# Kernel tuning notes

Hardware: AMD Instinct MI355X
Metric: run time of the kernel (lower is better)

The kernel has to match this reference:

```python
import jax, jax.numpy as jnp
import numpy as np

N_VARS = 32
D_MODEL = 256
D_MECH = 128
D_NOISE = D_MODEL // 4
N_LAYERS = 3
TEMP = 0.5
BATCH = 512


def gelu(x):
    return jax.nn.gelu(x, approximate=False)  # torch nn.GELU default is exact erf


def setup_inputs() -> dict:
    key = jax.random.key(0)
    ks = jax.random.split(key, 12)
    n, d, m, dn = N_VARS, D_MODEL, D_MECH, D_NOISE
    return {
        "exogenous_noise": jax.random.normal(ks[0], (BATCH, n, dn), dtype=jnp.float32),
        # learned params (edge_logits init randn*0.5 for a nontrivial adjacency)
        "edge_logits": jax.random.normal(ks[1], (n, n), dtype=jnp.float32) * 0.5,
        "var_emb": jax.random.normal(ks[2], (n, d), dtype=jnp.float32) * 0.02,
        # shared parent_aggregate Linear(d, d); weights stored [in, out]
        "pa_W": jax.random.normal(ks[3], (d, d), dtype=jnp.float32) / np.sqrt(d).astype(np.float32),
        "pa_b": jnp.zeros((d,), dtype=jnp.float32),
        # per-variable mechanism MLP weights, stacked on variable axis
        "m_W1": jax.random.normal(ks[4], (n, d, m), dtype=jnp.float32) / np.sqrt(d).astype(np.float32),
        "m_b1": jnp.zeros((n, m), dtype=jnp.float32),
        "m_W2": jax.random.normal(ks[5], (n, m, m), dtype=jnp.float32) / np.sqrt(m).astype(np.float32),
        "m_b2": jnp.zeros((n, m), dtype=jnp.float32),
        "m_W3": jax.random.normal(ks[6], (n, m, d), dtype=jnp.float32) / np.sqrt(m).astype(np.float32),
        "m_b3": jnp.zeros((n, d), dtype=jnp.float32),
        # per-variable noise encoder Linear(dn, d)
        "ne_W": jax.random.normal(ks[7], (n, dn, d), dtype=jnp.float32) / np.sqrt(dn).astype(np.float32),
        "ne_b": jnp.zeros((n, d), dtype=jnp.float32),
    }


def _forward(exogenous_noise, edge_logits, var_emb, pa_W, pa_b,
             m_W1, m_b1, m_W2, m_b2, m_W3, m_b3, ne_W, ne_b):
    n, d = N_VARS, D_MODEL
    batch = exogenous_noise.shape[0]
    # eval-mode adjacency: sigmoid(masked_logits / temp); diagonal masked out
    diag_mask = 1.0 - jnp.eye(n, dtype=edge_logits.dtype)
    adj = jax.nn.sigmoid((edge_logits * diag_mask) / jnp.asarray(TEMP, edge_logits.dtype))
    adj_cols = adj.T                                  # row i = adj[:, i], parents of var i
    noise_t = jnp.transpose(exogenous_noise, (1, 0, 2))  # (n, batch, dn)

    values0 = jnp.zeros((batch, n, d), dtype=exogenous_noise.dtype)
    idx = jnp.arange(n)
    xs = (idx, adj_cols, var_emb, noise_t, m_W1, m_b1, m_W2, m_b2, m_W3, m_b3, ne_W, ne_b)

    def var_step(values, x):
        i, a_col, emb_i, nz, w1, b1, w2, b2, w3, b3, nw, nb = x
        # adjacency-weighted aggregation over ALL current values (sequentially updated)
        pc = jnp.einsum('v,bvd->bd', a_col, values)
        parent_input = gelu((pc + emb_i) @ pa_W + pa_b)
        h = gelu(parent_input @ w1 + b1)
        h = gelu(h @ w2 + b2)
        out = h @ w3 + b3
        out = out + gelu(nz @ nw + nb)               # noise encoder contribution
        values = values.at[:, i].set(out)
        return values, None

    values = values0
    for _ in range(N_LAYERS):
        values, _ = jax.lax.scan(var_step, values, xs)
    return values


def reference(exogenous_noise, edge_logits, var_emb, pa_W, pa_b,
              m_W1, m_b1, m_W2, m_b2, m_W3, m_b3, ne_W, ne_b):
    return _forward(exogenous_noise, edge_logits, var_emb, pa_W, pa_b,
                    m_W1, m_b1, m_W2, m_b2, m_W3, m_b3, ne_W, ne_b)
```

## Files before the change

kernel.cpp:

```cpp
#include <hip/hip_runtime.h>


typedef __bf16 bf16x8 __attribute__((ext_vector_type(8)));
typedef float  f32x4  __attribute__((ext_vector_type(4)));

#define N_VARS 32
#define BTILE 4
#define NBLK 128

#define WS_ADJB   0
#define WS_B3P    4096
#define WS_EMBP   36864
#define WS_WSB    69632
#define ELOFF_PA  0
#define ELOFF_W1  65536
#define ELOFF_W2  1114112
#define ELOFF_W3  1638400
#define ELOFF_W3P 2686976
#define WS_H2B    7540736

#define XSTR 272
#define HSTR 144
#define VSTR 40

__device__ __forceinline__ unsigned short f2b(float f) {
    unsigned u = __float_as_uint(f);
    u += 0x7FFFu + ((u >> 16) & 1u);
    return (unsigned short)(u >> 16);
}

__device__ __forceinline__ float b2f(unsigned short u) {
    return __uint_as_float(((unsigned)u) << 16);
}

__device__ __forceinline__ void bar_lds() {
    asm volatile("s_waitcnt lgkmcnt(0)\n\ts_barrier" ::: "memory");
}

__device__ __forceinline__ float gelu_e(float x) {
    float z  = x * 0.7071067811865476f;
    float az = fabsf(z);
    float t  = __builtin_amdgcn_rcpf(1.0f + 0.47047f * az);
    float p  = t * (0.3480242f + t * (-0.0958798f + t * 0.7478556f));
    float e  = 1.0f - p * __expf(-z * z);
    float er = (z < 0.0f) ? -e : e;
    return 0.5f * x * (1.0f + er);
}

__device__ __forceinline__ float pickq(f32x4 v, int q) {
    float lo = (q & 1) ? v[1] : v[0];
    float hi = (q & 1) ? v[3] : v[2];
    return (q & 2) ? hi : lo;
}

#define MFMA16(a, b, c) __builtin_amdgcn_mfma_f32_16x16x32_bf16(a, b, c, 0, 0, 0)

#define GLD4(dst, ptr) asm volatile("global_load_dwordx4 %0, %1, off" \
                                    : "=v"(dst) : "v"(ptr))
#define GLD1(dst, ptr) asm volatile("global_load_dword %0, %1, off" \
                                    : "=v"(dst) : "v"(ptr))

__global__ void prep_all(const float* __restrict__ paW, const float* __restrict__ mW1,
                         const float* __restrict__ mW2, const float* __restrict__ mW3,
                         const float* __restrict__ edge, unsigned short* __restrict__ wsb,
                         unsigned short* __restrict__ adjb,
                         const float* __restrict__ noise, const float* __restrict__ neW,
                         const float* __restrict__ neb, float* __restrict__ outp,
                         const float* __restrict__ mb3, const float* __restrict__ emb,
                         const float* __restrict__ pab,
                         float* __restrict__ b3P, float* __restrict__ embP) {
    __shared__ unsigned short tile[32 * 256];
    const int c = blockIdx.x, tid = threadIdx.x;
    if (c < 520) {
        const float* src; unsigned short* dst; int N, KS, ks;
        if (c < 8)        { src = paW;                     dst = wsb + ELOFF_PA;             N = 256; KS = 8; ks = c; }
        else if (c < 264) { int v = (c - 8) >> 3;   ks = (c - 8) & 7;
                            src = mW1 + v * 32768;         dst = wsb + ELOFF_W1 + v * 32768; N = 128; KS = 8; }
        else if (c < 392) { int v = (c - 264) >> 2; ks = (c - 264) & 3;
                            src = mW2 + v * 16384;         dst = wsb + ELOFF_W2 + v * 16384; N = 128; KS = 4; }
        else              { int v = (c - 392) >> 2; ks = (c - 392) & 3;
                            src = mW3 + v * 32768;         dst = wsb + ELOFF_W3 + v * 32768; N = 256; KS = 4; }
        const int kb = ks * 32, nsh = (N == 256) ? 8 : 7;
        for (int t = tid; t < 32 * N; t += 256) {
            int r = t >> nsh, col = t & (N - 1);
            tile[r * N + col] = f2b(src[(kb + r) * N + col]);
        }
        __syncthreads();
        const int nout = (N >> 4) * 64;
        for (int o = tid; o < nout; o += 256) {
            int nt = o >> 6, lane = o & 63;
            int n = nt * 16 + (lane & 15), k0 = (lane >> 4) << 3;
            unsigned e[8];
            #pragma unroll
            for (int j = 0; j < 8; j++) e[j] = tile[(k0 + j) * N + n];
            uint4 pk;
            pk.x = e[0] | (e[1] << 16); pk.y = e[2] | (e[3] << 16);
            pk.z = e[4] | (e[5] << 16); pk.w = e[6] | (e[7] << 16);
            *(uint4*)(dst + ((nt * KS + ks) * 64 + lane) * 8) = pk;
        }
    } else if (c == 520) {
        for (int t = tid; t < 1024; t += 256) {
            int v = t >> 5, ci = t & 31;
            float x = edge[t];
            float m = (v == ci) ? 0.0f : x;
            float a = __builtin_amdgcn_rcpf(1.0f + __expf(-2.0f * m));
            unsigned short hi = f2b(a);
            float rem = a - b2f(hi);
            adjb[ci * 64 + v]      = hi;
            adjb[ci * 64 + 32 + v] = f2b(rem);
        }
    } else if (c < 1545) {
        int sb = c - 521;
        int i = sb >> 5, g = sb & 31, d = tid;
        float w[64];
        #pragma unroll
        for (int k = 0; k < 64; k++) w[k] = neW[(i * 64 + k) * 256 + d];
        float bias = neb[i * 256 + d];
        for (int bb = 0; bb < 16; bb++) {
            int b = g * 16 + bb;
            const float* nr = noise + (b * 32 + i) * 64;
            float a0 = bias, a1 = 0.f, a2 = 0.f, a3 = 0.f;
            #pragma unroll
            for (int k = 0; k < 16; k++) {
                a0 += nr[4 * k + 0] * w[4 * k + 0];
                a1 += nr[4 * k + 1] * w[4 * k + 1];
                a2 += nr[4 * k + 2] * w[4 * k + 2];
                a3 += nr[4 * k + 3] * w[4 * k + 3];
            }
            outp[(b * 32 + i) * 256 + d] = gelu_e((a0 + a1) + (a2 + a3));
        }
    } else if (c < 2057) {
        const int idx = c - 1545;
        const int v = idx >> 4, mg = (idx & 15) * 8;
        const int d = tid;
        const float* w3r = mW3 + (size_t)(v * 128 + mg) * 256;
        float acc[8];
        #pragma unroll
        for (int r = 0; r < 8; r++) acc[r] = 0.f;
        for (int n = 0; n < 256; n++) {
            float pa = paW[n * 256 + d];
            #pragma unroll
            for (int r = 0; r < 8; r++) acc[r] += w3r[r * 256 + n] * pa;
        }
        const int ks = mg >> 5, lg = (mg >> 3) & 3;
        const int nt = d >> 4, lane = lg * 16 + (d & 15);
        uint4 pk;
        pk.x = (unsigned)f2b(acc[0]) | ((unsigned)f2b(acc[1]) << 16);
        pk.y = (unsigned)f2b(acc[2]) | ((unsigned)f2b(acc[3]) << 16);
        pk.z = (unsigned)f2b(acc[4]) | ((unsigned)f2b(acc[5]) << 16);
        pk.w = (unsigned)f2b(acc[6]) | ((unsigned)f2b(acc[7]) << 16);
        *(uint4*)(wsb + ELOFF_W3P + v * 32768 + ((nt * 4 + ks) * 64 + lane) * 8) = pk;
    } else if (c < 2089) {
        const int v = c - 2057;
        float a = 0.f;
        for (int n = 0; n < 256; n++) a += mb3[v * 256 + n] * paW[n * 256 + tid];
        b3P[v * 256 + tid] = a;
    } else {
        const int v = c - 2089;
        float a = pab[tid];
        for (int n = 0; n < 256; n++) a += emb[v * 256 + n] * paW[n * 256 + tid];
        embP[v * 256 + tid] = a;
    }
}

__global__ __launch_bounds__(512, 2) void
scm_main(const float* __restrict__ embP, const float* __restrict__ b3Pp,
         const float* __restrict__ mb1, const float* __restrict__ mb2,
         const unsigned short* __restrict__ adjb,
         const __bf16* __restrict__ wsbf, const float* __restrict__ outp,
         unsigned short* __restrict__ h2buf) {
    __shared__ unsigned short valsP[1024 * VSTR];
    __shared__ unsigned short ne2S[4 * 32 * 256];
    __shared__ unsigned short adjS[2048];
    __shared__ unsigned short X2[4 * XSTR];
    __shared__ unsigned short Hs1[4 * HSTR];
    __shared__ unsigned short Hs2[4 * HSTR];

    const int tid = threadIdx.x, blk = blockIdx.x;

    {
        uint4 z; z.x = z.y = z.z = z.w = 0;
        for (int k = tid; k < 5120; k += 512) ((uint4*)valsP)[k] = z;
        for (int k = tid; k < 1024; k += 512)
            ((unsigned*)adjS)[k] = ((const unsigned*)adjb)[k];
    }

    const int wid = tid >> 6, lane = tid & 63, l15 = lane & 15, q = lane >> 4;
    const int l3 = l15 & 3;
    const int nW = wid * 16 + l15;
    const int n0 = nW, n1 = nW + 128;

    {
        const int R = wid * 16 + l15;
        const float* src = outp + ((size_t)(blk * BTILE + (R >> 5)) * 32 + (R & 31)) * 256 + q * 8;
        bf16x8 afr[8];
        #pragma unroll
        for (int ks = 0; ks < 8; ks++) {
            float4 x0 = *(const float4*)(src + ks * 32);
            float4 x1 = *(const float4*)(src + ks * 32 + 4);
            uint4 pk;
            pk.x = (unsigned)f2b(x0.x) | ((unsigned)f2b(x0.y) << 16);
            pk.y = (unsigned)f2b(x0.z) | ((unsigned)f2b(x0.w) << 16);
            pk.z = (unsigned)f2b(x1.x) | ((unsigned)f2b(x1.y) << 16);
            pk.w = (unsigned)f2b(x1.z) | ((unsigned)f2b(x1.w) << 16);
            afr[ks] = __builtin_bit_cast(bf16x8, pk);
        }
        #pragma unroll 4
        for (int nt = 0; nt < 16; nt++) {
            f32x4 e4 = {0, 0, 0, 0}, o4 = {0, 0, 0, 0};
            #pragma unroll
            for (int ks = 0; ks < 8; ks += 2) {
                bf16x8 b0 = *(const bf16x8*)(wsbf + ELOFF_PA + ((nt * 8 + ks) * 64 + lane) * 8);
                bf16x8 b1 = *(const bf16x8*)(wsbf + ELOFF_PA + ((nt * 8 + ks + 1) * 64 + lane) * 8);
                e4 = MFMA16(afr[ks], b0, e4);
                o4 = MFMA16(afr[ks + 1], b1, o4);
            }
            f32x4 a = e4 + o4;
            #pragma unroll
            for (int rr = 0; rr < 4; rr++) {
                int R2 = wid * 16 + q * 4 + rr;
                ne2S[R2 * 256 + nt * 16 + l15] =
                    f2b(a[rr] + b3Pp[(R2 & 31) * 256 + nt * 16 + l15]);
            }
        }
    }

    X2[q * XSTR + n0] = f2b(gelu_e(embP[n0]));
    X2[q * XSTR + n1] = f2b(gelu_e(embP[n1]));
    bar_lds();

    struct WSet {
        uint4 w1[8]; uint4 w2[4]; uint4 p0[4]; uint4 p1[4];
        float s0, s1, s2, s3;
    };

    auto issue_set = [&](WSet& S, int st) {
        const int it = st & 31, nt2 = (st + 1) & 31;
        const __bf16* b1 = wsbf + ELOFF_W1 + (size_t)it * 32768 +
                           ((size_t)(wid * 8) * 64 + lane) * 8;
        #pragma unroll
        for (int ks = 0; ks < 8; ks++) GLD4(S.w1[ks], b1 + ks * 512);
        const __bf16* b2 = wsbf + ELOFF_W2 + (size_t)it * 16384 +
                           ((size_t)(wid * 4) * 64 + lane) * 8;
        #pragma unroll
        for (int ks = 0; ks < 4; ks++) GLD4(S.w2[ks], b2 + ks * 512);
        const __bf16* bp = wsbf + ELOFF_W3P + (size_t)it * 32768 +
                           ((size_t)(wid * 4) * 64 + lane) * 8;
        #pragma unroll
        for (int ks = 0; ks < 4; ks++) GLD4(S.p0[ks], bp + ks * 512);
        const __bf16* bq = bp + 16384;
        #pragma unroll
        for (int ks = 0; ks < 4; ks++) GLD4(S.p1[ks], bq + ks * 512);
        GLD1(S.s0, mb1 + it * 128 + nW);
        GLD1(S.s1, mb2 + it * 128 + nW);
        GLD1(S.s2, embP + nt2 * 256 + n0);
        GLD1(S.s3, embP + nt2 * 256 + n1);
    };

    auto step = [&](int s, const WSet& cur, WSet& nxt) {
        const int i = s & 31, ni = (s + 1) & 31;
        const bool last = s >= 64;

        issue_set(nxt, s + 1);
        asm volatile("s_waitcnt vmcnt(24)");
        __builtin_amdgcn_sched_barrier(0);

        const float ne2_0 = b2f(ne2S[(q * 32 + i) * 256 + n0]);
        const float ne2_1 = b2f(ne2S[(q * 32 + i) * 256 + n1]);
        bf16x8 anh = *(const bf16x8*)(adjS + ni * 64 + q * 8);
        bf16x8 anl = *(const bf16x8*)(adjS + ni * 64 + 32 + q * 8);
        const float ani = b2f(adjS[ni * 64 + i]) + b2f(adjS[ni * 64 + 32 + i]);

        {
            f32x4 aa = {0, 0, 0, 0}, ab = {0, 0, 0, 0};
            f32x4 ac = {0, 0, 0, 0}, ad = {0, 0, 0, 0};
            #pragma unroll
            for (int ks = 0; ks < 8; ks += 4) {
                bf16x8 af0 = *(const bf16x8*)(X2 + l3 * XSTR + ks * 32 + q * 8);
                bf16x8 af1 = *(const bf16x8*)(X2 + l3 * XSTR + (ks + 1) * 32 + q * 8);
                bf16x8 af2 = *(const bf16x8*)(X2 + l3 * XSTR + (ks + 2) * 32 + q * 8);
                bf16x8 af3 = *(const bf16x8*)(X2 + l3 * XSTR + (ks + 3) * 32 + q * 8);
                aa = MFMA16(af0, __builtin_bit_cast(bf16x8, cur.w1[ks]), aa);
                ab = MFMA16(af1, __builtin_bit_cast(bf16x8, cur.w1[ks + 1]), ab);
                ac = MFMA16(af2, __builtin_bit_cast(bf16x8, cur.w1[ks + 2]), ac);
                ad = MFMA16(af3, __builtin_bit_cast(bf16x8, cur.w1[ks + 3]), ad);
            }
            float sb = (pickq(aa, q) + pickq(ab, q)) +
                       (pickq(ac, q) + pickq(ad, q)) + cur.s0;
            Hs1[q * HSTR + nW] = f2b(gelu_e(sb));
        }
        bar_lds();

        float pc0 = 0.f, pc1 = 0.f, oP0, oP1;
        {
            f32x4 ca = {0, 0, 0, 0}, cb = {0, 0, 0, 0};
            #pragma unroll
            for (int ks = 0; ks < 4; ks += 2) {
                bf16x8 af0 = *(const bf16x8*)(Hs1 + l3 * HSTR + ks * 32 + q * 8);
                bf16x8 af1 = *(const bf16x8*)(Hs1 + l3 * HSTR + (ks + 1) * 32 + q * 8);
                ca = MFMA16(af0, __builtin_bit_cast(bf16x8, cur.w2[ks]), ca);
                cb = MFMA16(af1, __builtin_bit_cast(bf16x8, cur.w2[ks + 1]), cb);
            }
            #pragma unroll
            for (int t = 0; t < 4; t++) {
                bf16x8 vf0 = *(const bf16x8*)(valsP + (t * 256 + n0) * VSTR + q * 8);
                bf16x8 vf1 = *(const bf16x8*)(valsP + (t * 256 + n1) * VSTR + q * 8);
                f32x4 z = {0, 0, 0, 0};
                f32x4 p0 = MFMA16(anl, vf0, MFMA16(anh, vf0, z));
                f32x4 p1 = MFMA16(anl, vf1, MFMA16(anh, vf1, z));
                pc0 = (q == t) ? p0[0] : pc0;
                pc1 = (q == t) ? p1[0] : pc1;
            }
            oP0 = b2f(valsP[(q * 256 + n0) * VSTR + i]);
            oP1 = b2f(valsP[(q * 256 + n1) * VSTR + i]);
            float scv = pickq(ca, q) + pickq(cb, q) + cur.s1;
            unsigned short hv = f2b(gelu_e(scv));
            Hs2[q * HSTR + nW] = hv;
            if (last)
                h2buf[((size_t)i * 512 + blk * BTILE + q) * 128 + nW] = hv;
        }
        bar_lds();

        {
            f32x4 c0a = {0, 0, 0, 0}, c0b = {0, 0, 0, 0};
            f32x4 c1a = {0, 0, 0, 0}, c1b = {0, 0, 0, 0};
            #pragma unroll
            for (int ks = 0; ks < 4; ks += 2) {
                bf16x8 af0 = *(const bf16x8*)(Hs2 + l3 * HSTR + ks * 32 + q * 8);
                bf16x8 af1 = *(const bf16x8*)(Hs2 + l3 * HSTR + (ks + 1) * 32 + q * 8);
                c0a = MFMA16(af0, __builtin_bit_cast(bf16x8, cur.p0[ks]), c0a);
                c1a = MFMA16(af0, __builtin_bit_cast(bf16x8, cur.p1[ks]), c1a);
                c0b = MFMA16(af1, __builtin_bit_cast(bf16x8, cur.p0[ks + 1]), c0b);
                c1b = MFMA16(af1, __builtin_bit_cast(bf16x8, cur.p1[ks + 1]), c1b);
            }
            float nP0 = pickq(c0a, q) + pickq(c0b, q) + ne2_0;
            float nP1 = pickq(c1a, q) + pickq(c1b, q) + ne2_1;
            unsigned short ur0 = f2b(nP0), ur1 = f2b(nP1);
            valsP[(q * 256 + n0) * VSTR + i] = ur0;
            valsP[(q * 256 + n1) * VSTR + i] = ur1;
            float x0 = pc0 + ani * (b2f(ur0) - oP0) + cur.s2;
            float x1 = pc1 + ani * (b2f(ur1) - oP1) + cur.s3;
            X2[q * XSTR + n0] = f2b(gelu_e(x0));
            X2[q * XSTR + n1] = f2b(gelu_e(x1));
        }
        bar_lds();
    };

    WSet A, B;
    issue_set(A, 0);
    asm volatile("s_waitcnt vmcnt(0)");
    __builtin_amdgcn_sched_barrier(0);
    for (int ss = 0; ss < 48; ss++) {
        step(2 * ss,     A, B);
        step(2 * ss + 1, B, A);
    }
}

__global__ __launch_bounds__(256) void
post_out(const unsigned short* __restrict__ h2buf, const __bf16* __restrict__ wsbf,
         const float* __restrict__ mb3, float* __restrict__ outp) {
    const int tid = threadIdx.x;
    const int wid = tid >> 6, lane = tid & 63, l15 = lane & 15, q = lane >> 4;
    const int gid = blockIdx.x * 4 + wid;
    const int i = gid >> 5, bt = gid & 31;
    bf16x8 af[4];
    #pragma unroll
    for (int ks = 0; ks < 4; ks++)
        af[ks] = *(const bf16x8*)(h2buf + ((size_t)i * 512 + bt * 16 + l15) * 128 +
                                  ks * 32 + q * 8);
    #pragma unroll 4
    for (int nt = 0; nt < 16; nt++) {
        f32x4 e4 = {0, 0, 0, 0}, o4 = {0, 0, 0, 0};
        #pragma unroll
        for (int ks = 0; ks < 4; ks += 2) {
            bf16x8 b0 = *(const bf16x8*)(wsbf + ELOFF_W3 + (size_t)i * 32768 +
                                         ((nt * 4 + ks) * 64 + lane) * 8);
            bf16x8 b1 = *(const bf16x8*)(wsbf + ELOFF_W3 + (size_t)i * 32768 +
                                         ((nt * 4 + ks + 1) * 64 + lane) * 8);
            e4 = MFMA16(af[ks], b0, e4);
            o4 = MFMA16(af[ks + 1], b1, o4);
        }
        f32x4 a = e4 + o4;
        float bv = mb3[i * 256 + nt * 16 + l15];
        #pragma unroll
        for (int rr = 0; rr < 4; rr++) {
            int b = bt * 16 + q * 4 + rr;
            size_t o = ((size_t)b * 32 + i) * 256 + nt * 16 + l15;
            outp[o] = a[rr] + bv + outp[o];
        }
    }
}

extern "C" void kernel_launch(void* const* d_in, const int* in_sizes, int n_in,
                              void* d_out, int out_size, void* d_ws, size_t ws_size,
                              hipStream_t stream) {
    (void)in_sizes; (void)n_in; (void)out_size; (void)ws_size;
    const float* noise = (const float*)d_in[0];
    const float* edge  = (const float*)d_in[1];
    const float* emb   = (const float*)d_in[2];
    const float* paW   = (const float*)d_in[3];
    const float* pab   = (const float*)d_in[4];
    const float* mW1   = (const float*)d_in[5];
    const float* mb1   = (const float*)d_in[6];
    const float* mW2   = (const float*)d_in[7];
    const float* mb2   = (const float*)d_in[8];
    const float* mW3   = (const float*)d_in[9];
    const float* mb3   = (const float*)d_in[10];
    const float* neW   = (const float*)d_in[11];
    const float* neb   = (const float*)d_in[12];
    float* outp = (float*)d_out;

    unsigned short* adjb = (unsigned short*)((char*)d_ws + WS_ADJB);
    float* b3P  = (float*)((char*)d_ws + WS_B3P);
    float* embP = (float*)((char*)d_ws + WS_EMBP);
    unsigned short* wsb  = (unsigned short*)((char*)d_ws + WS_WSB);
    unsigned short* h2b  = (unsigned short*)((char*)d_ws + WS_H2B);

    prep_all<<<2121, 256, 0, stream>>>(paW, mW1, mW2, mW3, edge, wsb, adjb,
                                       noise, neW, neb, outp, mb3, emb, pab,
                                       b3P, embP);
    scm_main<<<NBLK, 512, 0, stream>>>(embP, b3P, mb1, mb2, adjb,
                                       (const __bf16*)wsb, outp, h2b);
    post_out<<<256, 256, 0, stream>>>(h2b, (const __bf16*)wsb, mb3, outp);
}
```

Baseline: 386.4 us.

## Fuse final output projection into last layer of main recurrent kernel

Removes the separate post_out kernel and the h2buf staging buffer by computing the W3 projection, bias and noise-residual add inside scm_main's final-layer steps. The last 32 steps become an unpipelined loop that loads all weights, including W3, directly each step. This saves a launch and a global write/read of hidden states. In exchange it loses the weight prefetch overlap for those steps and raises register pressure.

```diff
diff --git a/kernel.cpp b/kernel.cpp
--- a/kernel.cpp
+++ b/kernel.cpp
@@ -17,7 +17,6 @@
 #define ELOFF_W2  1114112
 #define ELOFF_W3  1638400
 #define ELOFF_W3P 2686976
-#define WS_H2B    7540736
 
 #define XSTR 272
 #define HSTR 144
@@ -166,9 +165,8 @@
 __global__ __launch_bounds__(512, 2) void
 scm_main(const float* __restrict__ embP, const float* __restrict__ b3Pp,
          const float* __restrict__ mb1, const float* __restrict__ mb2,
-         const unsigned short* __restrict__ adjb,
-         const __bf16* __restrict__ wsbf, const float* __restrict__ outp,
-         unsigned short* __restrict__ h2buf) {
+         const float* __restrict__ mb3, const unsigned short* __restrict__ adjb,
+         const __bf16* __restrict__ wsbf, float* __restrict__ outp) {
     __shared__ unsigned short valsP[1024 * VSTR];
     __shared__ unsigned short ne2S[4 * 32 * 256];
     __shared__ unsigned short adjS[2048];
@@ -257,9 +255,8 @@
         GLD1(S.s3, embP + nt2 * 256 + n1);
     };
 
-    auto step = [&](int s, const WSet& cur, WSet& nxt) {
+    auto stepA = [&](int s, const WSet& cur, WSet& nxt) {
         const int i = s & 31, ni = (s + 1) & 31;
-        const bool last = s >= 64;
 
         issue_set(nxt, s + 1);
         asm volatile("s_waitcnt vmcnt(24)");
@@ -314,10 +311,7 @@
             oP0 = b2f(valsP[(q * 256 + n0) * VSTR + i]);
             oP1 = b2f(valsP[(q * 256 + n1) * VSTR + i]);
             float scv = pickq(ca, q) + pickq(cb, q) + cur.s1;
-            unsigned short hv = f2b(gelu_e(scv));
-            Hs2[q * HSTR + nW] = hv;
-            if (last)
-                h2buf[((size_t)i * 512 + blk * BTILE + q) * 128 + nW] = hv;
+            Hs2[q * HSTR + nW] = f2b(gelu_e(scv));
         }
         bar_lds();
 
@@ -350,44 +344,134 @@
     issue_set(A, 0);
     asm volatile("s_waitcnt vmcnt(0)");
     __builtin_amdgcn_sched_barrier(0);
-    for (int ss = 0; ss < 48; ss++) {
-        step(2 * ss,     A, B);
-        step(2 * ss + 1, B, A);
+    for (int ss = 0; ss < 32; ss++) {
+        stepA(2 * ss,     A, B);
+        stepA(2 * ss + 1, B, A);
     }
-}
-
-__global__ __launch_bounds__(256) void
-post_out(const unsigned short* __restrict__ h2buf, const __bf16* __restrict__ wsbf,
-         const float* __restrict__ mb3, float* __restrict__ outp) {
-    const int tid = threadIdx.x;
-    const int wid = tid >> 6, lane = tid & 63, l15 = lane & 15, q = lane >> 4;
-    const int gid = blockIdx.x * 4 + wid;
-    const int i = gid >> 5, bt = gid & 31;
-    bf16x8 af[4];
-    #pragma unroll
-    for (int ks = 0; ks < 4; ks++)
-        af[ks] = *(const bf16x8*)(h2buf + ((size_t)i * 512 + bt * 16 + l15) * 128 +
-                                  ks * 32 + q * 8);
-    #pragma unroll 4
-    for (int nt = 0; nt < 16; nt++) {
-        f32x4 e4 = {0, 0, 0, 0}, o4 = {0, 0, 0, 0};
-        #pragma unroll
-        for (int ks = 0; ks < 4; ks += 2) {
-            bf16x8 b0 = *(const bf16x8*)(wsbf + ELOFF_W3 + (size_t)i * 32768 +
-                                         ((nt * 4 + ks) * 64 + lane) * 8);
-            bf16x8 b1 = *(const bf16x8*)(wsbf + ELOFF_W3 + (size_t)i * 32768 +
-                                         ((nt * 4 + ks + 1) * 64 + lane) * 8);
-            e4 = MFMA16(af[ks], b0, e4);
-            o4 = MFMA16(af[ks + 1], b1, o4);
-        }
-        f32x4 a = e4 + o4;
-        float bv = mb3[i * 256 + nt * 16 + l15];
-        #pragma unroll
-        for (int rr = 0; rr < 4; rr++) {
-            int b = bt * 16 + q * 4 + rr;
-            size_t o = ((size_t)b * 32 + i) * 256 + nt * 16 + l15;
-            outp[o] = a[rr] + bv + outp[o];
-        }
+    asm volatile("s_waitcnt vmcnt(0)");
+    __builtin_amdgcn_sched_barrier(0);
+
+    for (int s = 64; s < 96; s++) {
+        const int i = s & 31, ni = (s + 1) & 31;
+
+        float bi1 = mb1[i * 128 + nW];
+        float bi2 = mb2[i * 128 + nW];
+        bf16x8 w1f[8];
+        #pragma unroll
+        for (int ks = 0; ks < 8; ks++)
+            w1f[ks] = *(const bf16x8*)(wsbf + ELOFF_W1 + (size_t)i * 32768 +
+                                       ((wid * 8 + ks) * 64 + lane) * 8);
+        bf16x8 w2f[4], wPf0[4], wPf1[4], w3f0[4], w3f1[4];
+        #pragma unroll
+        for (int ks = 0; ks < 4; ks++) {
+            w2f[ks]  = *(const bf16x8*)(wsbf + ELOFF_W2 + (size_t)i * 16384 +
+                                        ((wid * 4 + ks) * 64 + lane) * 8);
+            wPf0[ks] = *(const bf16x8*)(wsbf + ELOFF_W3P + (size_t)i * 32768 +
+                                        ((wid * 4 + ks) * 64 + lane) * 8);
+            wPf1[ks] = *(const bf16x8*)(wsbf + ELOFF_W3P + (size_t)i * 32768 +
+                                        (((wid + 8) * 4 + ks) * 64 + lane) * 8);
+            w3f0[ks] = *(const bf16x8*)(wsbf + ELOFF_W3 + (size_t)i * 32768 +
+                                        ((wid * 4 + ks) * 64 + lane) * 8);
+            w3f1[ks] = *(const bf16x8*)(wsbf + ELOFF_W3 + (size_t)i * 32768 +
+                                        (((wid + 8) * 4 + ks) * 64 + lane) * 8);
+        }
+        const size_t nrow = ((size_t)(blk * BTILE + q) * 32 + i) * 256;
+        const float neq0 = outp[nrow + n0];
+        const float neq1 = outp[nrow + n1];
+        const float b3a = mb3[i * 256 + n0];
+        const float b3b = mb3[i * 256 + n1];
+        const float eP0 = embP[ni * 256 + n0];
+        const float eP1 = embP[ni * 256 + n1];
+        const float ne2_0 = b2f(ne2S[(q * 32 + i) * 256 + n0]);
+        const float ne2_1 = b2f(ne2S[(q * 32 + i) * 256 + n1]);
+        bf16x8 anh = *(const bf16x8*)(adjS + ni * 64 + q * 8);
+        bf16x8 anl = *(const bf16x8*)(adjS + ni * 64 + 32 + q * 8);
+        const float ani = b2f(adjS[ni * 64 + i]) + b2f(adjS[ni * 64 + 32 + i]);
+
+        {
+            f32x4 aa = {0, 0, 0, 0}, ab = {0, 0, 0, 0};
+            f32x4 ac = {0, 0, 0, 0}, ad = {0, 0, 0, 0};
+            #pragma unroll
+            for (int ks = 0; ks < 8; ks += 4) {
+                bf16x8 af0 = *(const bf16x8*)(X2 + l3 * XSTR + ks * 32 + q * 8);
+                bf16x8 af1 = *(const bf16x8*)(X2 + l3 * XSTR + (ks + 1) * 32 + q * 8);
+                bf16x8 af2 = *(const bf16x8*)(X2 + l3 * XSTR + (ks + 2) * 32 + q * 8);
+                bf16x8 af3 = *(const bf16x8*)(X2 + l3 * XSTR + (ks + 3) * 32 + q * 8);
+                aa = MFMA16(af0, w1f[ks], aa);
+                ab = MFMA16(af1, w1f[ks + 1], ab);
+                ac = MFMA16(af2, w1f[ks + 2], ac);
+                ad = MFMA16(af3, w1f[ks + 3], ad);
+            }
+            float sb = (pickq(aa, q) + pickq(ab, q)) +
+                       (pickq(ac, q) + pickq(ad, q)) + bi1;
+            Hs1[q * HSTR + nW] = f2b(gelu_e(sb));
+        }
+        bar_lds();
+
+        float pc0 = 0.f, pc1 = 0.f, oP0, oP1;
+        {
+            f32x4 ca = {0, 0, 0, 0}, cb = {0, 0, 0, 0};
+            #pragma unroll
+            for (int ks = 0; ks < 4; ks += 2) {
+                bf16x8 af0 = *(const bf16x8*)(Hs1 + l3 * HSTR + ks * 32 + q * 8);
+                bf16x8 af1 = *(const bf16x8*)(Hs1 + l3 * HSTR + (ks + 1) * 32 + q * 8);
+                ca = MFMA16(af0, w2f[ks], ca);
+                cb = MFMA16(af1, w2f[ks + 1], cb);
+            }
+            #pragma unroll
+            for (int t = 0; t < 4; t++) {
+                bf16x8 vf0 = *(const bf16x8*)(valsP + (t * 256 + n0) * VSTR + q * 8);
+                bf16x8 vf1 = *(const bf16x8*)(valsP + (t * 256 + n1) * VSTR + q * 8);
+                f32x4 z = {0, 0, 0, 0};
+                f32x4 p0 = MFMA16(anl, vf0, MFMA16(anh, vf0, z));
+                f32x4 p1 = MFMA16(anl, vf1, MFMA16(anh, vf1, z));
+                pc0 = (q == t) ? p0[0] : pc0;
+                pc1 = (q == t) ? p1[0] : pc1;
+            }
+            oP0 = b2f(valsP[(q * 256 + n0) * VSTR + i]);
+            oP1 = b2f(valsP[(q * 256 + n1) * VSTR + i]);
+            float scv = pickq(ca, q) + pickq(cb, q) + bi2;
+            Hs2[q * HSTR + nW] = f2b(gelu_e(scv));
+        }
+        bar_lds();
+
+        {
+            f32x4 c0a = {0, 0, 0, 0}, c0b = {0, 0, 0, 0};
+            f32x4 c1a = {0, 0, 0, 0}, c1b = {0, 0, 0, 0};
+            #pragma unroll
+            for (int ks = 0; ks < 4; ks += 2) {
+                bf16x8 af0 = *(const bf16x8*)(Hs2 + l3 * HSTR + ks * 32 + q * 8);
+                bf16x8 af1 = *(const bf16x8*)(Hs2 + l3 * HSTR + (ks + 1) * 32 + q * 8);
+                c0a = MFMA16(af0, wPf0[ks], c0a);
+                c1a = MFMA16(af0, wPf1[ks], c1a);
+                c0b = MFMA16(af1, wPf0[ks + 1], c0b);
+                c1b = MFMA16(af1, wPf1[ks + 1], c1b);
+            }
+            float nP0 = pickq(c0a, q) + pickq(c0b, q) + ne2_0;
+            float nP1 = pickq(c1a, q) + pickq(c1b, q) + ne2_1;
+            unsigned short ur0 = f2b(nP0), ur1 = f2b(nP1);
+            valsP[(q * 256 + n0) * VSTR + i] = ur0;
+            valsP[(q * 256 + n1) * VSTR + i] = ur1;
+            float x0 = pc0 + ani * (b2f(ur0) - oP0) + eP0;
+            float x1 = pc1 + ani * (b2f(ur1) - oP1) + eP1;
+            X2[q * XSTR + n0] = f2b(gelu_e(x0));
+            X2[q * XSTR + n1] = f2b(gelu_e(x1));
+
+            f32x4 d0a = {0, 0, 0, 0}, d0b = {0, 0, 0, 0};
+            f32x4 d1a = {0, 0, 0, 0}, d1b = {0, 0, 0, 0};
+            #pragma unroll
+            for (int ks = 0; ks < 4; ks += 2) {
+                bf16x8 af0 = *(const bf16x8*)(Hs2 + l3 * HSTR + ks * 32 + q * 8);
+                bf16x8 af1 = *(const bf16x8*)(Hs2 + l3 * HSTR + (ks + 1) * 32 + q * 8);
+                d0a = MFMA16(af0, w3f0[ks], d0a);
+                d1a = MFMA16(af0, w3f1[ks], d1a);
+                d0b = MFMA16(af1, w3f0[ks + 1], d0b);
+                d1b = MFMA16(af1, w3f1[ks + 1], d1b);
+            }
+            outp[nrow + n0] = pickq(d0a, q) + pickq(d0b, q) + b3a + neq0;
+            outp[nrow + n1] = pickq(d1a, q) + pickq(d1b, q) + b3b + neq1;
+        }
+        bar_lds();
     }
 }
 
@@ -414,12 +498,10 @@
     float* b3P  = (float*)((char*)d_ws + WS_B3P);
     float* embP = (float*)((char*)d_ws + WS_EMBP);
     unsigned short* wsb  = (unsigned short*)((char*)d_ws + WS_WSB);
-    unsigned short* h2b  = (unsigned short*)((char*)d_ws + WS_H2B);
 
     prep_all<<<2121, 256, 0, stream>>>(paW, mW1, mW2, mW3, edge, wsb, adjb,
                                        noise, neW, neb, outp, mb3, emb, pab,
                                        b3P, embP);
-    scm_main<<<NBLK, 512, 0, stream>>>(embP, b3P, mb1, mb2, adjb,
-                                       (const __bf16*)wsb, outp, h2b);
-    post_out<<<256, 256, 0, stream>>>(h2b, (const __bf16*)wsb, mb3, outp);
-}
+    scm_main<<<NBLK, 512, 0, stream>>>(embP, b3P, mb1, mb2, mb3, adjb,
+                                       (const __bf16*)wsb, outp);
+}
```

Result: slower. 397.3 us (+2.8%).
